# Performance work log

Hardware: AMD Instinct MI355X
Metric: run time of the kernel (lower is better)

The kernel has to match this reference:

```python
import jax, jax.numpy as jnp
import numpy as np

NUM_LIMBS = 15
MSG_DIM = 32
MAX_CHILDREN = 2
STATE_DIM = 32
BATCH = 8192
# complete binary tree: children of node i are 2i+1, 2i+2
LEVELS = [[0], [1, 2], [3, 4, 5, 6], [7, 8, 9, 10, 11, 12, 13, 14]]


def _normalize(v, eps=1e-12):
    # F.normalize(v, dim=-1): v / max(||v||_2, eps)
    n = jnp.linalg.norm(v, axis=-1, keepdims=True)
    return v / jnp.maximum(n, eps)


def _linear(x, w, b):
    return x @ w.T + b


def _mlp(x, w1, b1, w2, b2, w3, b3):
    # MLPBase: Linear->ReLU->Linear->ReLU->Linear (hidden 400, 300)
    h = jax.nn.relu(_linear(x, w1, b1))
    h = jax.nn.relu(_linear(h, w2, b2))
    return _linear(h, w3, b3)


def setup_inputs() -> dict:
    key = jax.random.key(0)
    keys = iter(jax.random.split(key, 32))

    def p(shape, scale=0.05):
        return jax.random.normal(next(keys), shape, dtype=jnp.float32) * scale

    M2 = MSG_DIM * MAX_CHILDREN  # 64
    inp = {
        'x': jax.random.normal(next(keys), (NUM_LIMBS, BATCH, STATE_DIM), jnp.float32),
        'u': jax.random.normal(next(keys), (NUM_LIMBS, BATCH, 1), jnp.float32),
        # CriticUp (shared across limbs)
        'up_fc1_w': p((64, STATE_DIM + 1)), 'up_fc1_b': p((64,)),
        'up_fc2_w': p((64, 64 + M2)), 'up_fc2_b': p((64,)),
        'up_fc3_w': p((MSG_DIM, 64)), 'up_fc3_b': p((MSG_DIM,)),
        # CriticDownAction.baseQ1 / baseQ2: MLPBase(msg+act+msg, 1)
        'q1_l1_w': p((400, 2 * MSG_DIM + 1)), 'q1_l1_b': p((400,)),
        'q1_l2_w': p((300, 400)), 'q1_l2_b': p((300,)),
        'q1_l3_w': p((1, 300)), 'q1_l3_b': p((1,)),
        'q2_l1_w': p((400, 2 * MSG_DIM + 1)), 'q2_l1_b': p((400,)),
        'q2_l2_w': p((300, 400)), 'q2_l2_b': p((300,)),
        'q2_l3_w': p((1, 300)), 'q2_l3_b': p((1,)),
        # CriticDownAction.msg_base: MLPBase(msg+msg, msg*max_children)
        'mb_l1_w': p((400, 2 * MSG_DIM)), 'mb_l1_b': p((400,)),
        'mb_l2_w': p((300, 400)), 'mb_l2_b': p((300,)),
        'mb_l3_w': p((M2, 300)), 'mb_l3_b': p((M2,)),
    }
    return inp


def reference(x, u, up_fc1_w, up_fc1_b, up_fc2_w, up_fc2_b, up_fc3_w, up_fc3_b,
              q1_l1_w, q1_l1_b, q1_l2_w, q1_l2_b, q1_l3_w, q1_l3_b,
              q2_l1_w, q2_l1_b, q2_l2_w, q2_l2_b, q2_l3_w, q2_l3_b,
              mb_l1_w, mb_l1_b, mb_l2_w, mb_l2_b, mb_l3_w, mb_l3_b):
    B = x.shape[1]
    # ---- bottom-up pass: CriticUp per node, children messages concatenated ----
    msg_up = jnp.zeros((NUM_LIMBS, B, MSG_DIM), x.dtype)
    for level in reversed(LEVELS):
        idx = np.asarray(level)
        if 2 * idx[0] + 1 < NUM_LIMBS:  # static: this level has children
            m = jnp.concatenate([msg_up[2 * idx + 1], msg_up[2 * idx + 2]], axis=-1)
        else:
            m = jnp.zeros((len(idx), B, MSG_DIM * MAX_CHILDREN), x.dtype)
        xu = _normalize(_linear(jnp.concatenate([x[idx], u[idx]], -1), up_fc1_w, up_fc1_b))
        h = jnp.tanh(jnp.concatenate([xu, m], -1))
        h = jnp.tanh(_linear(h, up_fc2_w, up_fc2_b))
        msg_up = msg_up.at[idx].set(_normalize(_linear(h, up_fc3_w, up_fc3_b)))
    # ---- top-down pass: CriticDownAction(self_input = msg_up, action, parent msg) ----
    msg_in = jnp.zeros((NUM_LIMBS, B, MSG_DIM), x.dtype)
    q = jnp.zeros((NUM_LIMBS, B, 2), x.dtype)
    for level in LEVELS:
        idx = np.asarray(level)
        xs, us, ms = msg_up[idx], u[idx], msg_in[idx]
        xum = jnp.concatenate([xs, us, ms], -1)
        q1 = _mlp(xum, q1_l1_w, q1_l1_b, q1_l2_w, q1_l2_b, q1_l3_w, q1_l3_b)
        q2 = _mlp(xum, q2_l1_w, q2_l1_b, q2_l2_w, q2_l2_b, q2_l3_w, q2_l3_b)
        q = q.at[idx].set(jnp.concatenate([q1, q2], -1))
        xm = jnp.tanh(jnp.concatenate([xs, ms], -1))
        md = _normalize(_mlp(xm, mb_l1_w, mb_l1_b, mb_l2_w, mb_l2_b, mb_l3_w, mb_l3_b))
        if 2 * idx[0] + 1 < NUM_LIMBS:  # static: deliver per-child chunks
            md = md.reshape(len(idx), B, MAX_CHILDREN, MSG_DIM)
            msg_in = msg_in.at[2 * idx + 1].set(md[:, :, 0])
            msg_in = msg_in.at[2 * idx + 2].set(md[:, :, 1])
    return q  # [num_limbs, B, 2] = (Q1, Q2) per limb
```

## Files before the change

### kernel.cpp

```cpp
#include <hip/hip_runtime.h>
#include <hip/hip_bf16.h>

#define BN 8192
#define LOGB 13

typedef __attribute__((ext_vector_type(8))) short short8;
typedef __attribute__((ext_vector_type(4))) float f32x4;

__device__ __forceinline__ float tanh_fast(float x) {
  x = fminf(fmaxf(x, -15.f), 15.f);
  float t = __expf(2.f * x);
  return (t - 1.f) / (t + 1.f);
}

__device__ __forceinline__ unsigned short f2bf(float f) {
  union { __hip_bfloat16 h; unsigned short u; } cv;
  cv.h = __float2bfloat16(f);
  return cv.u;
}

__device__ __forceinline__ float bf2f(unsigned short s) {
  return __uint_as_float(((unsigned)s) << 16);
}

__device__ __forceinline__ uint2 pack4bf(float a, float b, float c, float d) {
  unsigned lo = (unsigned)f2bf(a) | ((unsigned)f2bf(b) << 16);
  unsigned hi = (unsigned)f2bf(c) | ((unsigned)f2bf(d) << 16);
  return make_uint2(lo, hi);
}

__device__ __forceinline__ void pack_one(
    const float* __restrict__ W, unsigned short* __restrict__ dst,
    int i, int Nsrc, int Ksrc, int nKs, int skip) {
  int j = i & 7, l = (i >> 3) & 63, fi = i >> 9;
  int ks = fi % nKs, nt = fi / nKs;
  int n = nt * 16 + (l & 15);
  int k = ks * 32 + ((l >> 4) << 3) + j;
  if (skip >= 0 && k >= skip) k++;
  float v = (n < Nsrc && k < Ksrc) ? W[n * Ksrc + k] : 0.f;
  dst[i] = f2bf(v);
}

__global__ __launch_bounds__(256) void k_prep_pack(
    const float* __restrict__ s0, unsigned short* __restrict__ d0,
    const float* __restrict__ s1, unsigned short* __restrict__ d1,
    const float* __restrict__ s2, unsigned short* __restrict__ d2,
    const float* __restrict__ s3, unsigned short* __restrict__ d3,
    const float* __restrict__ s4, unsigned short* __restrict__ d4,
    const float* __restrict__ s5, unsigned short* __restrict__ d5,
    const float* __restrict__ s6, unsigned short* __restrict__ d6,
    const float* __restrict__ s7, unsigned short* __restrict__ d7,
    const float* __restrict__ s8, unsigned short* __restrict__ d8,
    const float* __restrict__ s9, unsigned short* __restrict__ d9,
    float* __restrict__ wu0, float* __restrict__ wu1) {
  int i = blockIdx.x * 256 + threadIdx.x;
  if (i < 25600) { pack_one(s0, d0, i, 400, 65, 2, 32); return; }
  i -= 25600;
  if (i < 126464) { pack_one(s1, d1, i, 300, 400, 13, -1); return; }
  i -= 126464;
  if (i < 25600) { pack_one(s2, d2, i, 400, 65, 2, 32); return; }
  i -= 25600;
  if (i < 126464) { pack_one(s3, d3, i, 300, 400, 13, -1); return; }
  i -= 126464;
  if (i < 25600) { pack_one(s4, d4, i, 400, 64, 2, -1); return; }
  i -= 25600;
  if (i < 126464) { pack_one(s5, d5, i, 300, 400, 13, -1); return; }
  i -= 126464;
  if (i < 20480) { pack_one(s6, d6, i, 64, 300, 10, -1); return; }
  i -= 20480;
  if (i < 2048) { pack_one(s7, d7, i, 64, 33, 1, -1); return; }
  i -= 2048;
  if (i < 8192) { pack_one(s8, d8, i, 64, 128, 4, -1); return; }
  i -= 8192;
  if (i < 2048) { pack_one(s9, d9, i, 32, 64, 2, -1); return; }
  i -= 2048;
  if (i < 400) { wu0[i] = s0[i * 65 + 32]; return; }
  i -= 400;
  if (i < 400) { wu1[i] = s2[i * 65 + 32]; return; }
}

__global__ __launch_bounds__(512, 4) void k_up_mfma(
    const float* __restrict__ x, const float* __restrict__ u,
    const unsigned short* __restrict__ w1f, const float* __restrict__ w1raw,
    const float* __restrict__ b1,
    const unsigned short* __restrict__ w2f, const float* __restrict__ b2,
    const unsigned short* __restrict__ w3f, const float* __restrict__ b3,
    float* __restrict__ msg_up, int phase, int node_base) {
  __shared__ __align__(16) unsigned short Xs[64 * 40];
  __shared__ __align__(16) unsigned short Hs[64 * 136];
  __shared__ __align__(16) unsigned short H2s[64 * 72];
  __shared__ float Ms[2][64][32];
  __shared__ float Red[2][64];
  __shared__ float u_s[64];
  const int tid = threadIdx.x, w = tid >> 6, l = tid & 63;
  const int lr = l & 15, lh = l >> 4;
  const int mt = w & 3, nh = w >> 2;
  const int r0 = blockIdx.x * 64;
  const short8* w1v = (const short8*)w1f;
  const short8* w2v = (const short8*)w2f;
  const short8* w3v = (const short8*)w3f;

  const int nsteps = phase ? 1 : 3;
  const int sroot = 3 + blockIdx.y;

  for (int step = 0; step < nsteps; step++) {
    int node, sl = 0, sr = 0, os = -1;
    bool haveCh;
    if (phase) {
      node = node_base + blockIdx.y; haveCh = true;
    } else {
      switch (step) {
        case 0: node = 2 * sroot + 1; haveCh = false; os = 0; break;
        case 1: node = 2 * sroot + 2; haveCh = false; os = 1; break;
        default: node = sroot; haveCh = true; sl = 0; sr = 1; os = -1; break;
      }
    }
    const int rbase = (node << LOGB) + r0;

    for (int f = tid; f < 64 * 32; f += 512) {
      int r = f >> 5, c = f & 31;
      Xs[r * 40 + c] = f2bf(x[(rbase + r) * 32 + c]);
    }
    if (tid < 64) u_s[tid] = u[rbase + tid];
    if (haveCh) {
      for (int f = tid; f < 64 * 64; f += 512) {
        int r = f >> 6, c = f & 63;
        float v;
        if (phase)
          v = (c < 32) ? msg_up[(((2 * node + 1) << LOGB) + r0 + r) * 32 + c]
                       : msg_up[(((2 * node + 2) << LOGB) + r0 + r) * 32 + (c - 32)];
        else
          v = (c < 32) ? Ms[sl][r][c] : Ms[sr][r][c - 32];
        Hs[r * 136 + 64 + c] = f2bf(tanh_fast(v));
      }
    }
    __syncthreads();

    f32x4 acc1[2];
#pragma unroll
    for (int t = 0; t < 2; t++) acc1[t] = (f32x4)(0.f);
    {
      short8 a = *(const short8*)&Xs[(mt * 16 + lr) * 40 + lh * 8];
#pragma unroll
      for (int t = 0; t < 2; t++)
        acc1[t] = __builtin_amdgcn_mfma_f32_16x16x32_bf16(a, w1v[(nh * 2 + t) * 64 + l], acc1[t], 0, 0, 0);
    }
    float v1[2][4];
    {
      float vsq[4] = {0.f, 0.f, 0.f, 0.f};
#pragma unroll
      for (int t = 0; t < 2; t++) {
        int n = (nh * 2 + t) * 16 + lr;
        float wu = w1raw[n * 33 + 32];
        float bb = b1[n];
#pragma unroll
        for (int r = 0; r < 4; r++) {
          float vv = acc1[t][r] + u_s[mt * 16 + lh * 4 + r] * wu + bb;
          v1[t][r] = vv;
          vsq[r] += vv * vv;
        }
      }
#pragma unroll
      for (int r = 0; r < 4; r++) {
        float s = vsq[r];
        s += __shfl_xor(s, 1, 64);
        s += __shfl_xor(s, 2, 64);
        s += __shfl_xor(s, 4, 64);
        s += __shfl_xor(s, 8, 64);
        if (lr == 0) Red[nh][mt * 16 + lh * 4 + r] = s;
      }
    }
    __syncthreads();
#pragma unroll
    for (int r = 0; r < 4; r++) {
      int row = mt * 16 + lh * 4 + r;
      float inv = 1.f / fmaxf(sqrtf(Red[0][row] + Red[1][row]), 1e-12f);
#pragma unroll
      for (int t = 0; t < 2; t++)
        Hs[row * 136 + (nh * 2 + t) * 16 + lr] = f2bf(tanh_fast(v1[t][r] * inv));
    }
    __syncthreads();

    f32x4 acc2[2];
#pragma unroll
    for (int t = 0; t < 2; t++) acc2[t] = (f32x4)(0.f);
    const int ksmax = haveCh ? 4 : 2;
#pragma unroll
    for (int ks = 0; ks < 4; ks++) {
      if (ks < ksmax) {
        short8 a = *(const short8*)&Hs[(mt * 16 + lr) * 136 + ks * 32 + lh * 8];
#pragma unroll
        for (int t = 0; t < 2; t++)
          acc2[t] = __builtin_amdgcn_mfma_f32_16x16x32_bf16(a, w2v[((nh * 2 + t) * 4 + ks) * 64 + l], acc2[t], 0, 0, 0);
      }
    }
#pragma unroll
    for (int t = 0; t < 2; t++) {
      int n = (nh * 2 + t) * 16 + lr;
      float bb = b2[n];
#pragma unroll
      for (int r = 0; r < 4; r++)
        H2s[(mt * 16 + lh * 4 + r) * 72 + n] = f2bf(tanh_fast(acc2[t][r] + bb));
    }
    __syncthreads();

    f32x4 acc3 = (f32x4)(0.f);
#pragma unroll
    for (int ks = 0; ks < 2; ks++) {
      short8 a = *(const short8*)&H2s[(mt * 16 + lr) * 72 + ks * 32 + lh * 8];
      acc3 = __builtin_amdgcn_mfma_f32_16x16x32_bf16(a, w3v[(nh * 2 + ks) * 64 + l], acc3, 0, 0, 0);
    }
    float v3[4];
    {
      float bb = b3[nh * 16 + lr];
#pragma unroll
      for (int r = 0; r < 4; r++) {
        v3[r] = acc3[r] + bb;
        float s = v3[r] * v3[r];
        s += __shfl_xor(s, 1, 64);
        s += __shfl_xor(s, 2, 64);
        s += __shfl_xor(s, 4, 64);
        s += __shfl_xor(s, 8, 64);
        if (lr == 0) Red[nh][mt * 16 + lh * 4 + r] = s;
      }
    }
    __syncthreads();
    {
      const int n = nh * 16 + lr;
#pragma unroll
      for (int r = 0; r < 4; r++) {
        int row = mt * 16 + lh * 4 + r;
        float inv = 1.f / fmaxf(sqrtf(Red[0][row] + Red[1][row]), 1e-12f);
        float mv = v3[r] * inv;
        msg_up[(rbase + row) * 32 + n] = mv;
        if (os >= 0) Ms[os][row][n] = mv;
      }
    }
    __syncthreads();
  }
}

__global__ __launch_bounds__(512, 2) void k_mb_fused(
    const float* __restrict__ msg_up,
    const unsigned short* __restrict__ w1f, const unsigned short* __restrict__ w2f,
    const unsigned short* __restrict__ w3f,
    const float* __restrict__ b1, const float* __restrict__ b2, const float* __restrict__ b3,
    float* __restrict__ msg_in_out) {
  __shared__ __align__(16) unsigned short H1s[32 * 424];
  __shared__ __align__(16) unsigned short H2s[32 * 328];
  __shared__ __align__(16) unsigned short MinS[6][32][32];
  __shared__ __align__(16) unsigned char XR[32 * 72 * 2];
  unsigned short* Xs = (unsigned short*)XR;
  float* RedM = (float*)XR;
  const int tid = threadIdx.x;
  const int r0 = blockIdx.x * 32;
  const int w = tid >> 6, l = tid & 63;
  const int lr = l & 15, lh = l >> 4;
  const short8* w1v = (const short8*)w1f;
  const short8* w2v = (const short8*)w2f;
  const short8* w3v = (const short8*)w3f;

  for (int f = tid; f < 32 * 16; f += 512)
    H1s[(f >> 4) * 424 + 400 + (f & 15)] = 0;
  for (int f = tid; f < 32 * 16; f += 512)
    H2s[(f >> 4) * 328 + 304 + (f & 15)] = 0;

  for (int node = 0; node < 7; node++) {
    const int rbase = (node << LOGB) + r0;
    for (int f = tid; f < 32 * 64; f += 512) {
      int r = f >> 6, c = f & 63;
      float v;
      if (c < 32) v = msg_up[(rbase + r) * 32 + c];
      else v = (node > 0) ? bf2f(MinS[node - 1][r][c - 32]) : 0.f;
      Xs[r * 72 + c] = f2bf(tanh_fast(v));
    }
    __syncthreads();

    const int nb1 = (w == 0) ? 0 : (3 * w + 1);
    const int nc1 = (w == 0) ? 4 : 3;
    f32x4 acc1[4][2];
#pragma unroll
    for (int i = 0; i < 4; i++)
#pragma unroll
      for (int m = 0; m < 2; m++) acc1[i][m] = (f32x4)(0.f);
#pragma unroll
    for (int ks = 0; ks < 2; ks++) {
      short8 bx[2];
#pragma unroll
      for (int m = 0; m < 2; m++)
        bx[m] = *(const short8*)&Xs[(m * 16 + lr) * 72 + ks * 32 + lh * 8];
      short8 aw[4];
#pragma unroll
      for (int nt = 0; nt < 4; nt++)
        if (nt < nc1) aw[nt] = w1v[((nb1 + nt) * 2 + ks) * 64 + l];
#pragma unroll
      for (int nt = 0; nt < 4; nt++)
        if (nt < nc1)
#pragma unroll
          for (int m = 0; m < 2; m++)
            acc1[nt][m] = __builtin_amdgcn_mfma_f32_16x16x32_bf16(aw[nt], bx[m], acc1[nt][m], 0, 0, 0);
    }
#pragma unroll
    for (int nt = 0; nt < 4; nt++)
      if (nt < nc1) {
        int n0 = (nb1 + nt) * 16 + lh * 4;
        float4 bb = *(const float4*)&b1[n0];
#pragma unroll
        for (int m = 0; m < 2; m++) {
          float h0 = fmaxf(acc1[nt][m][0] + bb.x, 0.f);
          float h1 = fmaxf(acc1[nt][m][1] + bb.y, 0.f);
          float h2 = fmaxf(acc1[nt][m][2] + bb.z, 0.f);
          float h3 = fmaxf(acc1[nt][m][3] + bb.w, 0.f);
          *(uint2*)&H1s[(m * 16 + lr) * 424 + n0] = pack4bf(h0, h1, h2, h3);
        }
      }
    __syncthreads();

    const int nb2 = (w < 3) ? 3 * w : (9 + 2 * (w - 3));
    const int nc2 = (w < 3) ? 3 : 2;
    f32x4 acc2[3][2];
#pragma unroll
    for (int i = 0; i < 3; i++)
#pragma unroll
      for (int m = 0; m < 2; m++) acc2[i][m] = (f32x4)(0.f);
#pragma unroll 2
    for (int ks = 0; ks < 13; ks++) {
      short8 bh[2];
#pragma unroll
      for (int m = 0; m < 2; m++)
        bh[m] = *(const short8*)&H1s[(m * 16 + lr) * 424 + ks * 32 + lh * 8];
      short8 aw[3];
#pragma unroll
      for (int nt = 0; nt < 3; nt++)
        if (nt < nc2) aw[nt] = w2v[((nb2 + nt) * 13 + ks) * 64 + l];
#pragma unroll
      for (int nt = 0; nt < 3; nt++)
        if (nt < nc2)
#pragma unroll
          for (int m = 0; m < 2; m++)
            acc2[nt][m] = __builtin_amdgcn_mfma_f32_16x16x32_bf16(aw[nt], bh[m], acc2[nt][m], 0, 0, 0);
    }
#pragma unroll
    for (int nt = 0; nt < 3; nt++)
      if (nt < nc2) {
        int n0 = (nb2 + nt) * 16 + lh * 4;
        float b2v[4];
#pragma unroll
        for (int r = 0; r < 4; r++) {
          int n = n0 + r;
          b2v[r] = (n < 300) ? b2[n] : 0.f;
        }
#pragma unroll
        for (int m = 0; m < 2; m++) {
          float hv[4];
#pragma unroll
          for (int r = 0; r < 4; r++)
            hv[r] = (n0 + r < 300) ? fmaxf(acc2[nt][m][r] + b2v[r], 0.f) : 0.f;
          *(uint2*)&H2s[(m * 16 + lr) * 328 + n0] = pack4bf(hv[0], hv[1], hv[2], hv[3]);
        }
      }
    __syncthreads();

    float v3[2][4];
    if (w < 4) {
      f32x4 acc3[2];
#pragma unroll
      for (int m = 0; m < 2; m++) acc3[m] = (f32x4)(0.f);
#pragma unroll 2
      for (int ks = 0; ks < 10; ks++) {
        short8 bh[2];
#pragma unroll
        for (int m = 0; m < 2; m++)
          bh[m] = *(const short8*)&H2s[(m * 16 + lr) * 328 + ks * 32 + lh * 8];
        short8 aw = w3v[(w * 10 + ks) * 64 + l];
#pragma unroll
        for (int m = 0; m < 2; m++)
          acc3[m] = __builtin_amdgcn_mfma_f32_16x16x32_bf16(aw, bh[m], acc3[m], 0, 0, 0);
      }
      int n0 = w * 16 + lh * 4;
      float4 bb = *(const float4*)&b3[n0];
#pragma unroll
      for (int m = 0; m < 2; m++) {
        v3[m][0] = acc3[m][0] + bb.x;
        v3[m][1] = acc3[m][1] + bb.y;
        v3[m][2] = acc3[m][2] + bb.z;
        v3[m][3] = acc3[m][3] + bb.w;
        float ss = v3[m][0] * v3[m][0] + v3[m][1] * v3[m][1] +
                   v3[m][2] * v3[m][2] + v3[m][3] * v3[m][3];
        ss += __shfl_xor(ss, 16, 64);
        ss += __shfl_xor(ss, 32, 64);
        if (l < 16) RedM[w * 32 + m * 16 + l] = ss;
      }
    }
    __syncthreads();
    if (w < 4) {
      const int child = 2 * node + 1 + (w >> 1);
      const int ccol0 = (w & 1) * 16 + lh * 4;
#pragma unroll
      for (int m = 0; m < 2; m++) {
        const int row = m * 16 + lr;
        float ss = RedM[0 * 32 + row] + RedM[1 * 32 + row] + RedM[2 * 32 + row] + RedM[3 * 32 + row];
        float inv = 1.f / fmaxf(sqrtf(ss), 1e-12f);
        float4 o;
        o.x = v3[m][0] * inv; o.y = v3[m][1] * inv;
        o.z = v3[m][2] * inv; o.w = v3[m][3] * inv;
        *(float4*)&msg_in_out[((child << LOGB) + r0 + row) * 32 + ccol0] = o;
        if (child <= 6) *(uint2*)&MinS[child - 1][row][ccol0] = pack4bf(o.x, o.y, o.z, o.w);
      }
    }
    __syncthreads();
  }
}

__global__ __launch_bounds__(512, 4) void k_q_mfma(
    const float* __restrict__ msg_up, const float* __restrict__ u,
    const float* __restrict__ msg_in,
    const unsigned short* __restrict__ w1fA, const unsigned short* __restrict__ w2fA,
    const float* __restrict__ wuA, const float* __restrict__ b1A,
    const float* __restrict__ b2A, const float* __restrict__ w3A, const float* __restrict__ b3A,
    const unsigned short* __restrict__ w1fB, const unsigned short* __restrict__ w2fB,
    const float* __restrict__ wuB, const float* __restrict__ b1B,
    const float* __restrict__ b2B, const float* __restrict__ w3B, const float* __restrict__ b3B,
    float* __restrict__ out) {
  __shared__ __align__(16) unsigned char sraw[64 * 72 * 2];
  __shared__ __align__(16) unsigned short H1s[64 * 424];
  __shared__ float u_s[64];
  unsigned short* Xs = (unsigned short*)sraw;
  float* Red = (float*)sraw;

  const int tid = threadIdx.x;
  const int net = blockIdx.y;
  const unsigned short* w1f = net ? w1fB : w1fA;
  const unsigned short* w2f = net ? w2fB : w2fA;
  const float* wua = net ? wuB : wuA;
  const float* b1 = net ? b1B : b1A;
  const float* b2 = net ? b2B : b2A;
  const float* w3 = net ? w3B : w3A;
  const float* b3 = net ? b3B : b3A;
  const int r0 = blockIdx.x * 64;
  const int node = r0 >> LOGB;
  const int has_parent = (node > 0);
  const short8* w1v = (const short8*)w1f;
  const short8* w2v = (const short8*)w2f;

  {
    const int r = tid >> 3, seg = tid & 7;
    float4 v0, v1;
    if (seg < 4) {
      const float4* p = (const float4*)&msg_up[(r0 + r) * 32 + seg * 8];
      v0 = p[0]; v1 = p[1];
    } else if (has_parent) {
      const float4* p = (const float4*)&msg_in[(r0 + r) * 32 + (seg - 4) * 8];
      v0 = p[0]; v1 = p[1];
    } else {
      v0 = make_float4(0.f, 0.f, 0.f, 0.f); v1 = v0;
    }
    unsigned short tmp[8] = {f2bf(v0.x), f2bf(v0.y), f2bf(v0.z), f2bf(v0.w),
                             f2bf(v1.x), f2bf(v1.y), f2bf(v1.z), f2bf(v1.w)};
    *(short8*)&Xs[r * 72 + seg * 8] = *(const short8*)tmp;
  }
  for (int f = tid; f < 64 * 16; f += 512)
    H1s[(f >> 4) * 424 + 400 + (f & 15)] = 0;
  if (tid < 64) u_s[tid] = u[r0 + tid];
  __syncthreads();

  const int w = tid >> 6, l = tid & 63;
  const int lr = l & 15, lh = l >> 4;

  const int nb1 = (w == 0) ? 0 : (3 * w + 1);
  const int nc1 = (w == 0) ? 4 : 3;
  f32x4 acc1[4][4];
#pragma unroll
  for (int i = 0; i < 4; i++)
#pragma unroll
    for (int m = 0; m < 4; m++) acc1[i][m] = (f32x4)(0.f);
#pragma unroll
  for (int ks = 0; ks < 2; ks++) {
    short8 bx[4];
#pragma unroll
    for (int m = 0; m < 4; m++)
      bx[m] = *(const short8*)&Xs[(m * 16 + lr) * 72 + ks * 32 + lh * 8];
    short8 aw[4];
#pragma unroll
    for (int nt = 0; nt < 4; nt++)
      if (nt < nc1) aw[nt] = w1v[((nb1 + nt) * 2 + ks) * 64 + l];
#pragma unroll
    for (int nt = 0; nt < 4; nt++)
      if (nt < nc1)
#pragma unroll
        for (int m = 0; m < 4; m++)
          acc1[nt][m] = __builtin_amdgcn_mfma_f32_16x16x32_bf16(aw[nt], bx[m], acc1[nt][m], 0, 0, 0);
  }
#pragma unroll
  for (int nt = 0; nt < 4; nt++)
    if (nt < nc1) {
      int n0 = (nb1 + nt) * 16 + lh * 4;
      float4 bb = *(const float4*)&b1[n0];
      float4 wu = *(const float4*)&wua[n0];
#pragma unroll
      for (int m = 0; m < 4; m++) {
        float uv = u_s[m * 16 + lr];
        float h0 = fmaxf(acc1[nt][m][0] + uv * wu.x + bb.x, 0.f);
        float h1 = fmaxf(acc1[nt][m][1] + uv * wu.y + bb.y, 0.f);
        float h2 = fmaxf(acc1[nt][m][2] + uv * wu.z + bb.z, 0.f);
        float h3 = fmaxf(acc1[nt][m][3] + uv * wu.w + bb.w, 0.f);
        *(uint2*)&H1s[(m * 16 + lr) * 424 + n0] = pack4bf(h0, h1, h2, h3);
      }
    }
  __syncthreads();

  const int nb2 = (w < 3) ? 3 * w : (9 + 2 * (w - 3));
  const int nc2 = (w < 3) ? 3 : 2;
  f32x4 acc2[3][4];
#pragma unroll
  for (int i = 0; i < 3; i++)
#pragma unroll
    for (int m = 0; m < 4; m++) acc2[i][m] = (f32x4)(0.f);
#pragma unroll 2
  for (int ks = 0; ks < 13; ks++) {
    short8 bh[4];
#pragma unroll
    for (int m = 0; m < 4; m++)
      bh[m] = *(const short8*)&H1s[(m * 16 + lr) * 424 + ks * 32 + lh * 8];
    short8 aw[3];
#pragma unroll
    for (int nt = 0; nt < 3; nt++)
      if (nt < nc2) aw[nt] = w2v[((nb2 + nt) * 13 + ks) * 64 + l];
#pragma unroll
    for (int nt = 0; nt < 3; nt++)
      if (nt < nc2)
#pragma unroll
        for (int m = 0; m < 4; m++)
          acc2[nt][m] = __builtin_amdgcn_mfma_f32_16x16x32_bf16(aw[nt], bh[m], acc2[nt][m], 0, 0, 0);
  }
  float part[4];
#pragma unroll
  for (int m = 0; m < 4; m++) part[m] = 0.f;
#pragma unroll
  for (int nt = 0; nt < 3; nt++)
    if (nt < nc2) {
      int n0 = (nb2 + nt) * 16 + lh * 4;
      float b2v[4], w3v4[4];
#pragma unroll
      for (int r = 0; r < 4; r++) {
        int n = n0 + r;
        b2v[r] = (n < 300) ? b2[n] : 0.f;
        w3v4[r] = (n < 300) ? w3[n] : 0.f;
      }
#pragma unroll
      for (int m = 0; m < 4; m++)
#pragma unroll
        for (int r = 0; r < 4; r++) {
          float h = fmaxf(acc2[nt][m][r] + b2v[r], 0.f);
          part[m] = fmaf(h, w3v4[r], part[m]);
        }
    }
#pragma unroll
  for (int m = 0; m < 4; m++) {
    float p = part[m];
    p += __shfl_xor(p, 16, 64);
    p += __shfl_xor(p, 32, 64);
    if (l < 16) Red[w * 64 + m * 16 + l] = p;
  }
  __syncthreads();
  if (tid < 64) {
    float q = b3[0];
#pragma unroll
    for (int i = 0; i < 8; i++) q += Red[i * 64 + tid];
    out[(r0 + tid) * 2 + net] = q;
  }
}

extern "C" void kernel_launch(void* const* d_in, const int* in_sizes, int n_in,
                              void* d_out, int out_size, void* d_ws, size_t ws_size,
                              hipStream_t stream) {
  const float* x    = (const float*)d_in[0];
  const float* u    = (const float*)d_in[1];
  const float* up1w = (const float*)d_in[2];  const float* up1b = (const float*)d_in[3];
  const float* up2w = (const float*)d_in[4];  const float* up2b = (const float*)d_in[5];
  const float* up3w = (const float*)d_in[6];  const float* up3b = (const float*)d_in[7];
  const float* q1w1 = (const float*)d_in[8];  const float* q1b1 = (const float*)d_in[9];
  const float* q1w2 = (const float*)d_in[10]; const float* q1b2 = (const float*)d_in[11];
  const float* q1w3 = (const float*)d_in[12]; const float* q1b3 = (const float*)d_in[13];
  const float* q2w1 = (const float*)d_in[14]; const float* q2b1 = (const float*)d_in[15];
  const float* q2w2 = (const float*)d_in[16]; const float* q2b2 = (const float*)d_in[17];
  const float* q2w3 = (const float*)d_in[18]; const float* q2b3 = (const float*)d_in[19];
  const float* mbw1 = (const float*)d_in[20]; const float* mbb1 = (const float*)d_in[21];
  const float* mbw2 = (const float*)d_in[22]; const float* mbb2 = (const float*)d_in[23];
  const float* mbw3 = (const float*)d_in[24]; const float* mbb3 = (const float*)d_in[25];
  float* out = (float*)d_out;
  float* ws  = (float*)d_ws;

  float* msg_up = ws;
  float* msg_in = msg_up + 15 * BN * 32;
  unsigned short* frag = (unsigned short*)(msg_in + 15 * BN * 32);
  unsigned short* q1w1f = frag;
  unsigned short* q1w2f = q1w1f + 25600;
  unsigned short* q2w1f = q1w2f + 126464;
  unsigned short* q2w2f = q2w1f + 25600;
  unsigned short* mbw1f = q2w2f + 126464;
  unsigned short* mbw2f = mbw1f + 25600;
  unsigned short* mbw3f = mbw2f + 126464;
  unsigned short* up1f  = mbw3f + 20480;
  unsigned short* up2f  = up1f + 2048;
  unsigned short* up3f  = up2f + 8192;
  float* wuQ1 = (float*)(up3f + 2048);
  float* wuQ2 = wuQ1 + 400;

  k_prep_pack<<<dim3((489760 + 255) / 256), dim3(256), 0, stream>>>(
      q1w1, q1w1f, q1w2, q1w2f, q2w1, q2w1f, q2w2, q2w2f,
      mbw1, mbw1f, mbw2, mbw2f, mbw3, mbw3f,
      up1w, up1f, up2w, up2f, up3w, up3f, wuQ1, wuQ2);

  k_up_mfma<<<dim3(BN / 64, 4), dim3(512), 0, stream>>>(
      x, u, up1f, up1w, up1b, up2f, up2b, up3f, up3b, msg_up, 0, 0);
  k_up_mfma<<<dim3(BN / 64, 2), dim3(512), 0, stream>>>(
      x, u, up1f, up1w, up1b, up2f, up2b, up3f, up3b, msg_up, 1, 1);
  k_up_mfma<<<dim3(BN / 64, 1), dim3(512), 0, stream>>>(
      x, u, up1f, up1w, up1b, up2f, up2b, up3f, up3b, msg_up, 1, 0);

  k_mb_fused<<<dim3(BN / 32), dim3(512), 0, stream>>>(
      msg_up, mbw1f, mbw2f, mbw3f, mbb1, mbb2, mbb3, msg_in);

  k_q_mfma<<<dim3(15 * (BN / 64), 2), dim3(512), 0, stream>>>(
      msg_up, u, msg_in,
      q1w1f, q1w2f, wuQ1, q1b1, q1b2, q1w3, q1b3,
      q2w1f, q2w2f, wuQ2, q2b1, q2b2, q2w3, q2b3,
      out);
}
```

Baseline: 191.4 us.

## Spread msg-base layer 3 over all waves, drop MinS, add MFMA priority hints

```diff
diff --git a/kernel.cpp b/kernel.cpp
--- a/kernel.cpp
+++ b/kernel.cpp
@@ -248,7 +248,6 @@
     float* __restrict__ msg_in_out) {
   __shared__ __align__(16) unsigned short H1s[32 * 424];
   __shared__ __align__(16) unsigned short H2s[32 * 328];
-  __shared__ __align__(16) unsigned short MinS[6][32][32];
   __shared__ __align__(16) unsigned char XR[32 * 72 * 2];
   unsigned short* Xs = (unsigned short*)XR;
   float* RedM = (float*)XR;
@@ -271,7 +270,7 @@
       int r = f >> 6, c = f & 63;
       float v;
       if (c < 32) v = msg_up[(rbase + r) * 32 + c];
-      else v = (node > 0) ? bf2f(MinS[node - 1][r][c - 32]) : 0.f;
+      else v = (node > 0) ? msg_in_out[(rbase + r) * 32 + (c - 32)] : 0.f;
       Xs[r * 72 + c] = f2bf(tanh_fast(v));
     }
     __syncthreads();
@@ -283,6 +282,7 @@
     for (int i = 0; i < 4; i++)
 #pragma unroll
       for (int m = 0; m < 2; m++) acc1[i][m] = (f32x4)(0.f);
+    __builtin_amdgcn_s_setprio(1);
 #pragma unroll
     for (int ks = 0; ks < 2; ks++) {
       short8 bx[2];
@@ -300,6 +300,7 @@
           for (int m = 0; m < 2; m++)
             acc1[nt][m] = __builtin_amdgcn_mfma_f32_16x16x32_bf16(aw[nt], bx[m], acc1[nt][m], 0, 0, 0);
     }
+    __builtin_amdgcn_s_setprio(0);
 #pragma unroll
     for (int nt = 0; nt < 4; nt++)
       if (nt < nc1) {
@@ -323,6 +324,7 @@
     for (int i = 0; i < 3; i++)
 #pragma unroll
       for (int m = 0; m < 2; m++) acc2[i][m] = (f32x4)(0.f);
+    __builtin_amdgcn_s_setprio(1);
 #pragma unroll 2
     for (int ks = 0; ks < 13; ks++) {
       short8 bh[2];
@@ -340,6 +342,7 @@
           for (int m = 0; m < 2; m++)
             acc2[nt][m] = __builtin_amdgcn_mfma_f32_16x16x32_bf16(aw[nt], bh[m], acc2[nt][m], 0, 0, 0);
     }
+    __builtin_amdgcn_s_setprio(0);
 #pragma unroll
     for (int nt = 0; nt < 3; nt++)
       if (nt < nc2) {
@@ -361,52 +364,43 @@
       }
     __syncthreads();
 
-    float v3[2][4];
-    if (w < 4) {
-      f32x4 acc3[2];
-#pragma unroll
-      for (int m = 0; m < 2; m++) acc3[m] = (f32x4)(0.f);
+    float v3[4];
+    {
+      const int mL3 = w >> 2;
+      const int nt3 = w & 3;
+      f32x4 acc3 = (f32x4)(0.f);
+      __builtin_amdgcn_s_setprio(1);
 #pragma unroll 2
       for (int ks = 0; ks < 10; ks++) {
-        short8 bh[2];
-#pragma unroll
-        for (int m = 0; m < 2; m++)
-          bh[m] = *(const short8*)&H2s[(m * 16 + lr) * 328 + ks * 32 + lh * 8];
-        short8 aw = w3v[(w * 10 + ks) * 64 + l];
-#pragma unroll
-        for (int m = 0; m < 2; m++)
-          acc3[m] = __builtin_amdgcn_mfma_f32_16x16x32_bf16(aw, bh[m], acc3[m], 0, 0, 0);
-      }
-      int n0 = w * 16 + lh * 4;
+        short8 bh = *(const short8*)&H2s[(mL3 * 16 + lr) * 328 + ks * 32 + lh * 8];
+        short8 aw = w3v[(nt3 * 10 + ks) * 64 + l];
+        acc3 = __builtin_amdgcn_mfma_f32_16x16x32_bf16(aw, bh, acc3, 0, 0, 0);
+      }
+      __builtin_amdgcn_s_setprio(0);
+      int n0 = nt3 * 16 + lh * 4;
       float4 bb = *(const float4*)&b3[n0];
-#pragma unroll
-      for (int m = 0; m < 2; m++) {
-        v3[m][0] = acc3[m][0] + bb.x;
-        v3[m][1] = acc3[m][1] + bb.y;
-        v3[m][2] = acc3[m][2] + bb.z;
-        v3[m][3] = acc3[m][3] + bb.w;
-        float ss = v3[m][0] * v3[m][0] + v3[m][1] * v3[m][1] +
-                   v3[m][2] * v3[m][2] + v3[m][3] * v3[m][3];
-        ss += __shfl_xor(ss, 16, 64);
-        ss += __shfl_xor(ss, 32, 64);
-        if (l < 16) RedM[w * 32 + m * 16 + l] = ss;
-      }
-    }
-    __syncthreads();
-    if (w < 4) {
-      const int child = 2 * node + 1 + (w >> 1);
-      const int ccol0 = (w & 1) * 16 + lh * 4;
-#pragma unroll
-      for (int m = 0; m < 2; m++) {
-        const int row = m * 16 + lr;
-        float ss = RedM[0 * 32 + row] + RedM[1 * 32 + row] + RedM[2 * 32 + row] + RedM[3 * 32 + row];
-        float inv = 1.f / fmaxf(sqrtf(ss), 1e-12f);
-        float4 o;
-        o.x = v3[m][0] * inv; o.y = v3[m][1] * inv;
-        o.z = v3[m][2] * inv; o.w = v3[m][3] * inv;
-        *(float4*)&msg_in_out[((child << LOGB) + r0 + row) * 32 + ccol0] = o;
-        if (child <= 6) *(uint2*)&MinS[child - 1][row][ccol0] = pack4bf(o.x, o.y, o.z, o.w);
-      }
+      v3[0] = acc3[0] + bb.x;
+      v3[1] = acc3[1] + bb.y;
+      v3[2] = acc3[2] + bb.z;
+      v3[3] = acc3[3] + bb.w;
+      float ss = v3[0] * v3[0] + v3[1] * v3[1] + v3[2] * v3[2] + v3[3] * v3[3];
+      ss += __shfl_xor(ss, 16, 64);
+      ss += __shfl_xor(ss, 32, 64);
+      if (l < 16) RedM[nt3 * 32 + mL3 * 16 + l] = ss;
+    }
+    __syncthreads();
+    {
+      const int mL3 = w >> 2;
+      const int nt3 = w & 3;
+      const int row = mL3 * 16 + lr;
+      float ss = RedM[0 * 32 + row] + RedM[1 * 32 + row] + RedM[2 * 32 + row] + RedM[3 * 32 + row];
+      float inv = 1.f / fmaxf(sqrtf(ss), 1e-12f);
+      const int child = 2 * node + 1 + (nt3 >> 1);
+      const int ccol0 = (nt3 & 1) * 16 + lh * 4;
+      float4 o;
+      o.x = v3[0] * inv; o.y = v3[1] * inv;
+      o.z = v3[2] * inv; o.w = v3[3] * inv;
+      *(float4*)&msg_in_out[((child << LOGB) + r0 + row) * 32 + ccol0] = o;
     }
     __syncthreads();
   }
@@ -474,6 +468,7 @@
   for (int i = 0; i < 4; i++)
 #pragma unroll
     for (int m = 0; m < 4; m++) acc1[i][m] = (f32x4)(0.f);
+  __builtin_amdgcn_s_setprio(1);
 #pragma unroll
   for (int ks = 0; ks < 2; ks++) {
     short8 bx[4];
@@ -491,6 +486,7 @@
         for (int m = 0; m < 4; m++)
           acc1[nt][m] = __builtin_amdgcn_mfma_f32_16x16x32_bf16(aw[nt], bx[m], acc1[nt][m], 0, 0, 0);
   }
+  __builtin_amdgcn_s_setprio(0);
 #pragma unroll
   for (int nt = 0; nt < 4; nt++)
     if (nt < nc1) {
@@ -516,6 +512,7 @@
   for (int i = 0; i < 3; i++)
 #pragma unroll
     for (int m = 0; m < 4; m++) acc2[i][m] = (f32x4)(0.f);
+  __builtin_amdgcn_s_setprio(1);
 #pragma unroll 2
   for (int ks = 0; ks < 13; ks++) {
     short8 bh[4];
@@ -533,6 +530,7 @@
         for (int m = 0; m < 4; m++)
           acc2[nt][m] = __builtin_amdgcn_mfma_f32_16x16x32_bf16(aw[nt], bh[m], acc2[nt][m], 0, 0, 0);
   }
+  __builtin_amdgcn_s_setprio(0);
   float part[4];
 #pragma unroll
   for (int m = 0; m < 4; m++) part[m] = 0.f;
```

Measured after the change: 187.0 us, median of 2. 1.02x faster.
